# Performance work log

Measured on AMD Instinct MI355X. Metric: run time of the kernel, lower is better.

Reference implementation:

```python
import jax, jax.numpy as jnp
import numpy as np

B, N, C, H = 8, 1024, 1024, 16
D = C // H
DFF = 4 * C
EPS = 1e-6


def _ln(x):
    mu = jnp.mean(x, axis=-1, keepdims=True)
    var = jnp.mean(jnp.square(x - mu), axis=-1, keepdims=True)
    return (x - mu) / jnp.sqrt(var + EPS)


def _modulate(x, shift, scale):
    return x * (1 + scale) + shift


def setup_inputs() -> dict:
    key = jax.random.key(0)
    ks = jax.random.split(key, 12)
    s = 0.02
    inp = {
        "x": jax.random.normal(ks[0], (B, N, C), jnp.float32),
        "c": jax.random.normal(ks[1], (B, 1, C), jnp.float32),
        "causal_mask": jnp.tril(jnp.ones((N, N), jnp.int32))[None, None],  # [1,1,N,N]
        "qkv_w": jax.random.normal(ks[2], (3 * C, C), jnp.float32) * s,
        "qkv_b": jnp.zeros((3 * C,), jnp.float32),
        "proj_w": jax.random.normal(ks[3], (C, C), jnp.float32) * s,
        "proj_b": jnp.zeros((C,), jnp.float32),
        "fc1_w": jax.random.normal(ks[4], (DFF, C), jnp.float32) * s,
        "fc1_b": jnp.zeros((DFF,), jnp.float32),
        "fc2_w": jax.random.normal(ks[5], (C, DFF), jnp.float32) * s,
        "fc2_b": jnp.zeros((C,), jnp.float32),
        "ada_w": jax.random.normal(ks[6], (6 * C, C), jnp.float32) * s,
        "ada_b": jnp.zeros((6 * C,), jnp.float32),
    }
    return inp


def reference(x, c, causal_mask, qkv_w, qkv_b, proj_w, proj_b,
              fc1_w, fc1_b, fc2_w, fc2_b, ada_w, ada_b):
    # adaLN modulation: SiLU -> Linear(C -> 6C) -> chunk 6
    mod = jax.nn.silu(c) @ ada_w.T + ada_b  # [B,1,6C]
    (shift_msa, scale_msa, gate_msa,
     shift_mlp, scale_mlp, gate_mlp) = jnp.split(mod, 6, axis=-1)

    # --- causal attention ---
    y = _modulate(_ln(x), shift_msa, scale_msa)  # [B,N,C]
    qkv = y @ qkv_w.T + qkv_b                    # [B,N,3C]
    qkv = qkv.reshape(B, N, 3, H, D).transpose(2, 0, 3, 1, 4)  # [3,B,H,N,D]
    q, k, v = qkv[0], qkv[1], qkv[2]
    scale = D ** -0.5
    attn = jnp.einsum('bhnd,bhmd->bhnm', q, k) * scale  # [B,H,N,N]
    attn = jnp.where(causal_mask == 0, -jnp.inf, attn)
    attn = jax.nn.softmax(attn, axis=-1)
    o = jnp.einsum('bhnm,bhmd->bhnd', attn, v)
    o = o.transpose(0, 2, 1, 3).reshape(B, N, C)
    o = o @ proj_w.T + proj_b
    x = x + gate_msa * o

    # --- MLP ---
    z = _modulate(_ln(x), shift_mlp, scale_mlp)
    h = jax.nn.gelu(z @ fc1_w.T + fc1_b, approximate=True)
    m = h @ fc2_w.T + fc2_b
    x = x + gate_mlp * m
    return x
```

## Files before the change

kernel.cpp:

```cpp
#include <hip/hip_runtime.h>
#include <math.h>
#include <stdint.h>
#include <stddef.h>

namespace {

constexpr int kB = 8, kN = 1024, kC = 1024, kH = 16, kD = 64, kDFF = 4096;
constexpr int kM = kB * kN;
constexpr int k6C = 6 * kC;
constexpr float kQKScale = 0.18033688011112042f;
constexpr float kM8 = 8.0f;

typedef _Float16 half8 __attribute__((ext_vector_type(8)));
typedef _Float16 half4v __attribute__((ext_vector_type(4)));
typedef float f32x4 __attribute__((ext_vector_type(4)));
typedef int v4i __attribute__((ext_vector_type(4)));
typedef signed char i8;

__device__ inline void ld_lds16(const void* g, void* l) {
  __builtin_amdgcn_global_load_lds(
      (const __attribute__((address_space(1))) void*)g,
      (__attribute__((address_space(3))) void*)l, 16, 0, 0);
}

__device__ inline int xcd_swizzle(int flat, int nwg) {
  return (flat & 7) * (nwg >> 3) + (flat >> 3);
}

__device__ inline unsigned pack4_i8(float y0, float y1, float y2, float y3, float inv) {
  int q0 = (int)rintf(y0 * inv), q1 = (int)rintf(y1 * inv);
  int q2 = (int)rintf(y2 * inv), q3 = (int)rintf(y3 * inv);
  q0 = min(max(q0, -127), 127); q1 = min(max(q1, -127), 127);
  q2 = min(max(q2, -127), 127); q3 = min(max(q3, -127), 127);
  return (unsigned)(q0 & 0xFF) | ((unsigned)(q1 & 0xFF) << 8) |
         ((unsigned)(q2 & 0xFF) << 16) | ((unsigned)(q3 & 0xFF) << 24);
}

__global__ void cvt_f32_f16(const float* __restrict__ src, _Float16* __restrict__ dst) {
  size_t i = (size_t)blockIdx.x * 256 + threadIdx.x;
  float4 f = ((const float4*)src)[i];
  half4v h;
  h[0] = (_Float16)f.x; h[1] = (_Float16)f.y; h[2] = (_Float16)f.z; h[3] = (_Float16)f.w;
  ((half4v*)dst)[i] = h;
}

__global__ __launch_bounds__(256) void quant_w_kernel(
    const float* __restrict__ src, i8* __restrict__ dst, float* __restrict__ wscale) {
  int n = blockIdx.x, tid = threadIdx.x;
  const float* row = src + (size_t)n * kC;
  float4 f = ((const float4*)row)[tid];
  float m = fmaxf(fmaxf(fabsf(f.x), fabsf(f.y)), fmaxf(fabsf(f.z), fabsf(f.w)));
#pragma unroll
  for (int msk = 32; msk; msk >>= 1) m = fmaxf(m, __shfl_xor(m, msk));
  __shared__ float red[4];
  int w = tid >> 6, lane = tid & 63;
  if (lane == 0) red[w] = m;
  __syncthreads();
  m = fmaxf(fmaxf(red[0], red[1]), fmaxf(red[2], red[3]));
  m = fmaxf(m, 1e-12f);
  float inv = 127.f / m;
  ((unsigned*)(dst + (size_t)n * kC))[tid] = pack4_i8(f.x, f.y, f.z, f.w, inv);
  if (tid == 0) wscale[n] = m * (1.f / 127.f);
}

__global__ __launch_bounds__(256) void mod_kernel(
    const float* __restrict__ c, const float* __restrict__ ada_w,
    const float* __restrict__ ada_b, float* __restrict__ mod) {
  __shared__ float sc[kC];
  int b  = blockIdx.x / (k6C / 4);
  int j0 = (blockIdx.x % (k6C / 4)) * 4;
  int tid = threadIdx.x;
  for (int i = tid; i < kC; i += 256) {
    float v = c[b * kC + i];
    sc[i] = v / (1.f + expf(-v));
  }
  __syncthreads();
  int w = tid >> 6, lane = tid & 63;
  int j = j0 + w;
  const float* wr = ada_w + (size_t)j * kC;
  float acc = 0.f;
#pragma unroll
  for (int kk = 0; kk < kC / 64; ++kk) {
    int k = kk * 64 + lane;
    acc += sc[k] * wr[k];
  }
#pragma unroll
  for (int m = 32; m; m >>= 1) acc += __shfl_xor(acc, m);
  if (lane == 0) mod[b * k6C + j] = acc + ada_b[j];
}

template <typename T>
__global__ __launch_bounds__(256) void ln_mod_q_kernel(
    const T* __restrict__ x, const float* __restrict__ mod,
    i8* __restrict__ out, float* __restrict__ ascale,
    int shift_off, int scale_off) {
  int row = blockIdx.x;
  int b = row >> 10;
  const T* xr = x + (size_t)row * kC;
  int tid = threadIdx.x;
  int cc0 = tid * 4;
  float v[4];
  float s = 0.f, s2 = 0.f;
#pragma unroll
  for (int i = 0; i < 4; ++i) {
    v[i] = (float)xr[cc0 + i];
    s += v[i];
    s2 += v[i] * v[i];
  }
#pragma unroll
  for (int m = 32; m; m >>= 1) { s += __shfl_xor(s, m); s2 += __shfl_xor(s2, m); }
  __shared__ float red[8];
  __shared__ float redm[4];
  int w = tid >> 6, lane = tid & 63;
  if (lane == 0) { red[w] = s; red[4 + w] = s2; }
  __syncthreads();
  s  = red[0] + red[1] + red[2] + red[3];
  s2 = red[4] + red[5] + red[6] + red[7];
  float mu   = s * (1.f / kC);
  float var  = s2 * (1.f / kC) - mu * mu;
  float rstd = rsqrtf(var + 1e-6f);
  const float* mb = mod + (size_t)b * k6C;
  float y[4];
  float m = 0.f;
#pragma unroll
  for (int i = 0; i < 4; ++i) {
    y[i] = (v[i] - mu) * rstd * (1.f + mb[scale_off + cc0 + i]) + mb[shift_off + cc0 + i];
    m = fmaxf(m, fabsf(y[i]));
  }
#pragma unroll
  for (int msk = 32; msk; msk >>= 1) m = fmaxf(m, __shfl_xor(m, msk));
  if (lane == 0) redm[w] = m;
  __syncthreads();
  m = fmaxf(fmaxf(redm[0], redm[1]), fmaxf(redm[2], redm[3]));
  m = fmaxf(m, 1e-12f);
  float inv = 127.f / m;
  ((unsigned*)(out + (size_t)row * kC))[tid] = pack4_i8(y[0], y[1], y[2], y[3], inv);
  if (tid == 0) ascale[row] = m * (1.f / 127.f);
}

template <int EPI>
__global__ __launch_bounds__(256, 4) void gemm_i8_kernel(
    const i8* __restrict__ A, const i8* __restrict__ W,
    const float* __restrict__ ascale, const float* __restrict__ wscale,
    const float* __restrict__ bias, _Float16* __restrict__ outp,
    int M, int Nn, int K) {
  __shared__ __align__(16) i8 S[2 * 2 * 128 * 64];
  int tid = threadIdx.x;
  int nwg = (int)(gridDim.x * gridDim.y);
  int swz = xcd_swizzle((int)(blockIdx.y * gridDim.x + blockIdx.x), nwg);
  int bn = swz % (int)gridDim.x, bm = swz / (int)gridDim.x;
  int lane = tid & 63, w = tid >> 6;
  int l15 = lane & 15, quad = lane >> 4;
  int wr = (w >> 1) * 64, wc = (w & 1) * 64;

  v4i acc[4][4];
#pragma unroll
  for (int i = 0; i < 4; ++i)
#pragma unroll
    for (int j = 0; j < 4; ++j) acc[i][j] = (v4i){0, 0, 0, 0};

  const i8* Ag = A + (size_t)bm * 128 * K;
  const i8* Wg = W + (size_t)bn * 128 * K;
  int rg = lane >> 2;
  int gsl = lane & 3;

  int nk = K >> 6;
  {
    i8* As0 = S;
    i8* Bs0 = S + 128 * 64;
#pragma unroll
    for (int s = 0; s < 2; ++s) {
      int row = w * 32 + s * 16 + rg;
      int gc = (gsl ^ ((row >> 1) & 3)) * 16;
      ld_lds16(&Ag[(size_t)row * K + gc], &As0[(w * 32 + s * 16) * 64]);
      ld_lds16(&Wg[(size_t)row * K + gc], &Bs0[(w * 32 + s * 16) * 64]);
    }
  }
  __syncthreads();

  int cread = (quad ^ ((l15 >> 1) & 3)) * 16;
  for (int t = 0; t < nk; ++t) {
    const i8* As = S + (t & 1) * (2 * 128 * 64);
    const i8* Bs = As + 128 * 64;
    if (t + 1 < nk) {
      i8* Asn = S + ((t + 1) & 1) * (2 * 128 * 64);
      i8* Bsn = Asn + 128 * 64;
      int kt = (t + 1) << 6;
#pragma unroll
      for (int s = 0; s < 2; ++s) {
        int row = w * 32 + s * 16 + rg;
        int gc = (gsl ^ ((row >> 1) & 3)) * 16;
        ld_lds16(&Ag[(size_t)row * K + kt + gc], &Asn[(w * 32 + s * 16) * 64]);
        ld_lds16(&Wg[(size_t)row * K + kt + gc], &Bsn[(w * 32 + s * 16) * 64]);
      }
    }
    v4i af[4], bf[4];
#pragma unroll
    for (int i = 0; i < 4; ++i)
      af[i] = *(const v4i*)&As[(wr + i * 16 + l15) * 64 + cread];
#pragma unroll
    for (int j = 0; j < 4; ++j)
      bf[j] = *(const v4i*)&Bs[(wc + j * 16 + l15) * 64 + cread];
#pragma unroll
    for (int i = 0; i < 4; ++i)
#pragma unroll
      for (int j = 0; j < 4; ++j)
        acc[i][j] = __builtin_amdgcn_mfma_i32_16x16x64_i8(af[i], bf[j], acc[i][j], 0, 0, 0);
    __syncthreads();
  }

  _Float16* Cs = (_Float16*)S;
  int row0 = wr + quad * 4;
  int col0 = wc + l15;
#pragma unroll
  for (int i = 0; i < 4; ++i) {
#pragma unroll
    for (int j = 0; j < 4; ++j) {
      int colL = col0 + j * 16;
      int n = bn * 128 + colL;
      float ws = wscale[n];
      float bv = bias[n];
#pragma unroll
      for (int r = 0; r < 4; ++r) {
        int rowL = row0 + i * 16 + r;
        float as = ascale[bm * 128 + rowL];
        float v = (float)acc[i][j][r] * (as * ws) + bv;
        if constexpr (EPI == 0) {
          if (n < kC) v *= kQKScale;
        } else {
          float u = v + 0.044715f * v * v * v;
          float t = exp2f(-2.302208f * u);
          v = v * __builtin_amdgcn_rcpf(1.f + t);
        }
        Cs[rowL * 128 + (((colL >> 3) ^ (rowL & 7)) << 3) + (colL & 7)] = (_Float16)v;
      }
    }
  }
  __syncthreads();
#pragma unroll
  for (int p = 0; p < 8; ++p) {
    int r = (tid >> 4) + p * 16;
    int cc = tid & 15;
    half8 hv = *(const half8*)&Cs[r * 128 + ((cc ^ (r & 7)) << 3)];
    size_t gm = (size_t)(bm * 128 + r);
    int coff = bn * 128 + cc * 8;
    *(half8*)&outp[gm * Nn + coff] = hv;
  }
}

template <int EPI>
__global__ __launch_bounds__(256) void gemm_f16_kernel(
    const _Float16* __restrict__ A, const _Float16* __restrict__ W,
    const float* __restrict__ bias, void* __restrict__ outp,
    const void* __restrict__ resid, const float* __restrict__ mod,
    int M, int Nn, int K, int gate_off) {
  __shared__ __align__(16) _Float16 S[2 * 2 * 128 * 64];
  int tid = threadIdx.x;
  int nwg = (int)(gridDim.x * gridDim.y);
  int swz = xcd_swizzle((int)(blockIdx.y * gridDim.x + blockIdx.x), nwg);
  int bn = swz % (int)gridDim.x, bm = swz / (int)gridDim.x;
  int lane = tid & 63, w = tid >> 6;
  int l15 = lane & 15, quad = lane >> 4;
  int wr = (w >> 1) * 64, wc = (w & 1) * 64;

  f32x4 acc[4][4];
#pragma unroll
  for (int i = 0; i < 4; ++i)
#pragma unroll
    for (int j = 0; j < 4; ++j) acc[i][j] = (f32x4){0.f, 0.f, 0.f, 0.f};

  const _Float16* Ag = A + (size_t)bm * 128 * K;
  const _Float16* Wg = W + (size_t)bn * 128 * K;
  int r8 = lane >> 3;
  int jc = ((lane & 7) ^ r8) * 8;

  int nk = K / 64;
  {
    _Float16* Asp = S;
    _Float16* Bsp = S + 128 * 64;
#pragma unroll
    for (int u = 0; u < 4; ++u) {
      int row = w * 32 + u * 8 + r8;
      ld_lds16(&Ag[(size_t)row * K + jc], &Asp[(w * 32 + u * 8) * 64]);
      ld_lds16(&Wg[(size_t)row * K + jc], &Bsp[(w * 32 + u * 8) * 64]);
    }
  }
  __syncthreads();

  for (int t = 0; t < nk; ++t) {
    const _Float16* As = S + (t & 1) * (2 * 128 * 64);
    const _Float16* Bs = As + 128 * 64;
    if (t + 1 < nk) {
      _Float16* Asn = S + ((t + 1) & 1) * (2 * 128 * 64);
      _Float16* Bsn = Asn + 128 * 64;
      int kt = (t + 1) * 64;
#pragma unroll
      for (int u = 0; u < 4; ++u) {
        int row = w * 32 + u * 8 + r8;
        ld_lds16(&Ag[(size_t)row * K + kt + jc], &Asn[(w * 32 + u * 8) * 64]);
        ld_lds16(&Wg[(size_t)row * K + kt + jc], &Bsn[(w * 32 + u * 8) * 64]);
      }
    }
#pragma unroll
    for (int kk = 0; kk < 2; ++kk) {
      half8 af[4], bf[4];
#pragma unroll
      for (int i = 0; i < 4; ++i)
        af[i] = *(const half8*)&As[(wr + i * 16 + l15) * 64 +
                                   (((kk * 4 + quad) ^ (l15 & 7)) * 8)];
#pragma unroll
      for (int j = 0; j < 4; ++j)
        bf[j] = *(const half8*)&Bs[(wc + j * 16 + l15) * 64 +
                                   (((kk * 4 + quad) ^ (l15 & 7)) * 8)];
#pragma unroll
      for (int i = 0; i < 4; ++i)
#pragma unroll
        for (int j = 0; j < 4; ++j)
          acc[i][j] = __builtin_amdgcn_mfma_f32_16x16x32_f16(af[i], bf[j], acc[i][j], 0, 0, 0);
    }
    __syncthreads();
  }

  _Float16* Cs = S;
  int row0 = wr + quad * 4;
  int col0 = wc + l15;
#pragma unroll
  for (int i = 0; i < 4; ++i) {
#pragma unroll
    for (int j = 0; j < 4; ++j) {
      int colL = col0 + j * 16;
      int n = bn * 128 + colL;
      float bv = bias[n];
#pragma unroll
      for (int r = 0; r < 4; ++r) {
        int rowL = row0 + i * 16 + r;
        float v = acc[i][j][r] + bv;
        Cs[rowL * 128 + (((colL >> 3) ^ (rowL & 7)) << 3) + (colL & 7)] = (_Float16)v;
      }
    }
  }
  __syncthreads();
  int b6 = (bm >> 3) * k6C + gate_off + bn * 128;
#pragma unroll
  for (int p = 0; p < 8; ++p) {
    int r = (tid >> 4) + p * 16;
    int cc = tid & 15;
    half8 hv = *(const half8*)&Cs[r * 128 + ((cc ^ (r & 7)) << 3)];
    size_t gm = (size_t)(bm * 128 + r);
    int coff = bn * 128 + cc * 8;
    if constexpr (EPI == 2) {
      const float* rp = &((const float*)resid)[gm * kC + coff];
      const float* gp = &mod[b6 + cc * 8];
      half8 ov;
#pragma unroll
      for (int e = 0; e < 8; ++e) ov[e] = (_Float16)(rp[e] + gp[e] * (float)hv[e]);
      *(half8*)&((_Float16*)outp)[gm * kC + coff] = ov;
    } else {
      const _Float16* rp = &((const _Float16*)resid)[gm * kC + coff];
      const float* gp = &mod[b6 + cc * 8];
      half8 rv = *(const half8*)rp;
      float ov[8];
#pragma unroll
      for (int e = 0; e < 8; ++e) ov[e] = (float)rv[e] + gp[e] * (float)hv[e];
      *(float4*)&((float*)outp)[gm * kC + coff] = *(float4*)&ov[0];
      *(float4*)&((float*)outp)[gm * kC + coff + 4] = *(float4*)&ov[4];
    }
  }
}

__global__ __launch_bounds__(256) void vtrans_kernel(
    const _Float16* __restrict__ qkv, _Float16* __restrict__ vT) {
  int nt = blockIdx.x, h = blockIdx.y, b = blockIdx.z;
  __shared__ _Float16 Ts[64 * 72];
  int tid = threadIdx.x;
  const _Float16* src = qkv + ((size_t)(b * kN + nt * 64)) * (3 * kC) + 2 * kC + h * 64;
#pragma unroll
  for (int u = 0; u < 2; ++u) {
    int idx = tid + u * 256;
    int r = idx >> 3, c8 = (idx & 7) * 8;
    *(uint4*)&Ts[r * 72 + c8] = *(const uint4*)&src[(size_t)r * (3 * kC) + c8];
  }
  __syncthreads();
  _Float16* dst = vT + (((size_t)(b * kH + h)) * 64) * kN + nt * 64;
#pragma unroll
  for (int u = 0; u < 2; ++u) {
    int idx = tid + u * 256;
    int d = idx >> 3, n8 = (idx & 7) * 8;
    half8 v;
#pragma unroll
    for (int e = 0; e < 8; ++e) v[e] = Ts[(n8 + e) * 72 + d];
    *(half8*)&dst[(size_t)d * kN + n8] = v;
  }
}

__global__ __launch_bounds__(256) void attn_kernel(
    const _Float16* __restrict__ qkv, const _Float16* __restrict__ vT,
    _Float16* __restrict__ o) {
  int nwg = (int)(gridDim.x * gridDim.y * gridDim.z);
  int flat = (int)((blockIdx.z * gridDim.y + blockIdx.y) * gridDim.x + blockIdx.x);
  int swz = xcd_swizzle(flat, nwg);
  int qt = swz % (int)gridDim.x;
  int tmp = swz / (int)gridDim.x;
  int h = tmp % (int)gridDim.y, b = tmp / (int)gridDim.y;
  __shared__ __align__(16) _Float16 Qs[128 * 64];
  __shared__ __align__(16) _Float16 Ks[64 * 64];
  __shared__ __align__(16) _Float16 Vs[64 * 64];
  __shared__ __align__(16) _Float16 Ps[128 * 72];
  int tid = threadIdx.x, lane = tid & 63, w = tid >> 6;
  int l15 = lane & 15, quad = lane >> 4;
  int wq = w * 32;
  int r8 = lane >> 3;
  int jc = ((lane & 7) ^ r8) * 8;

  const _Float16* Qg = qkv + ((size_t)(b * kN + qt * 128)) * (3 * kC) + h * kD;
  const _Float16* Kg = qkv + ((size_t)(b * kN)) * (3 * kC) + kC + h * kD;
  const _Float16* Vg = vT + ((size_t)(b * kH + h) * kD) * kN;

#pragma unroll
  for (int u = 0; u < 4; ++u)
    ld_lds16(&Qg[(size_t)(w * 32 + u * 8 + r8) * (3 * kC) + jc],
             &Qs[(w * 32 + u * 8) * 64]);
  __syncthreads();

  half8 aq[2][2];
#pragma unroll
  for (int i = 0; i < 2; ++i)
#pragma unroll
    for (int kk = 0; kk < 2; ++kk)
      aq[i][kk] = *(const half8*)&Qs[(wq + i * 16 + l15) * 64 +
                                     (((kk * 4 + quad) ^ (l15 & 7)) * 8)];

  f32x4 o_acc[2][4];
  f32x4 lsum[2];
#pragma unroll
  for (int i = 0; i < 2; ++i) {
    lsum[i] = (f32x4){0.f, 0.f, 0.f, 0.f};
#pragma unroll
    for (int dt = 0; dt < 4; ++dt) o_acc[i][dt] = (f32x4){0.f, 0.f, 0.f, 0.f};
  }
  half8 ones;
#pragma unroll
  for (int e = 0; e < 8; ++e) ones[e] = (_Float16)1.f;

  int jmax = 2 * qt + 2;
  for (int j = 0; j < jmax; ++j) {
#pragma unroll
    for (int u = 0; u < 2; ++u) {
      int row = w * 16 + u * 8 + r8;
      ld_lds16(&Kg[(size_t)(j * 64 + row) * (3 * kC) + jc], &Ks[(w * 16 + u * 8) * 64]);
      ld_lds16(&Vg[(size_t)row * kN + j * 64 + jc],         &Vs[(w * 16 + u * 8) * 64]);
    }
    __syncthreads();
    bool need_mask = (j >= 2 * qt);

    f32x4 s[2][4];
#pragma unroll
    for (int ct = 0; ct < 4; ++ct) {
      half8 b0 = *(const half8*)&Ks[(ct * 16 + l15) * 64 + ((quad ^ (l15 & 7)) * 8)];
      half8 b1 = *(const half8*)&Ks[(ct * 16 + l15) * 64 + (((4 + quad) ^ (l15 & 7)) * 8)];
#pragma unroll
      for (int i = 0; i < 2; ++i) {
        f32x4 t = (f32x4){0.f, 0.f, 0.f, 0.f};
        t = __builtin_amdgcn_mfma_f32_16x16x32_f16(aq[i][0], b0, t, 0, 0, 0);
        t = __builtin_amdgcn_mfma_f32_16x16x32_f16(aq[i][1], b1, t, 0, 0, 0);
        s[i][ct] = t;
      }
    }

#pragma unroll
    for (int i = 0; i < 2; ++i)
#pragma unroll
      for (int ct = 0; ct < 4; ++ct)
#pragma unroll
        for (int r = 0; r < 4; ++r) {
          float p = exp2f(fminf(s[i][ct][r] - kM8, 14.f));
          if (need_mask) {
            int kg = j * 64 + ct * 16 + l15;
            int qg = qt * 128 + wq + i * 16 + quad * 4 + r;
            if (kg > qg) p = 0.f;
          }
          Ps[(wq + i * 16 + quad * 4 + r) * 72 + ct * 16 + l15] = (_Float16)p;
        }

    half8 ap[2][2];
#pragma unroll
    for (int i = 0; i < 2; ++i) {
      ap[i][0] = *(const half8*)&Ps[(wq + i * 16 + l15) * 72 + quad * 8];
      ap[i][1] = *(const half8*)&Ps[(wq + i * 16 + l15) * 72 + 32 + quad * 8];
      lsum[i] = __builtin_amdgcn_mfma_f32_16x16x32_f16(ap[i][0], ones, lsum[i], 0, 0, 0);
      lsum[i] = __builtin_amdgcn_mfma_f32_16x16x32_f16(ap[i][1], ones, lsum[i], 0, 0, 0);
    }
#pragma unroll
    for (int dt = 0; dt < 4; ++dt) {
      half8 bv0 = *(const half8*)&Vs[(dt * 16 + l15) * 64 + ((quad ^ (l15 & 7)) * 8)];
      half8 bv1 = *(const half8*)&Vs[(dt * 16 + l15) * 64 + (((4 + quad) ^ (l15 & 7)) * 8)];
#pragma unroll
      for (int i = 0; i < 2; ++i) {
        o_acc[i][dt] = __builtin_amdgcn_mfma_f32_16x16x32_f16(ap[i][0], bv0, o_acc[i][dt], 0, 0, 0);
        o_acc[i][dt] = __builtin_amdgcn_mfma_f32_16x16x32_f16(ap[i][1], bv1, o_acc[i][dt], 0, 0, 0);
      }
    }
    __syncthreads();
  }

#pragma unroll
  for (int i = 0; i < 2; ++i) {
    float rl[4];
#pragma unroll
    for (int r = 0; r < 4; ++r) rl[r] = __builtin_amdgcn_rcpf(lsum[i][r]);
#pragma unroll
    for (int dt = 0; dt < 4; ++dt)
#pragma unroll
      for (int r = 0; r < 4; ++r) {
        int q = qt * 128 + wq + i * 16 + quad * 4 + r;
        o[((size_t)(b * kN + q)) * kC + h * kD + dt * 16 + l15] =
            (_Float16)(o_acc[i][dt][r] * rl[r]);
      }
  }
}

}

extern "C" void kernel_launch(void* const* d_in, const int* in_sizes, int n_in,
                              void* d_out, int out_size, void* d_ws, size_t ws_size,
                              hipStream_t stream) {
  const float* x      = (const float*)d_in[0];
  const float* c      = (const float*)d_in[1];
  const float* qkv_w  = (const float*)d_in[3];
  const float* qkv_b  = (const float*)d_in[4];
  const float* proj_w = (const float*)d_in[5];
  const float* proj_b = (const float*)d_in[6];
  const float* fc1_w  = (const float*)d_in[7];
  const float* fc1_b  = (const float*)d_in[8];
  const float* fc2_w  = (const float*)d_in[9];
  const float* fc2_b  = (const float*)d_in[10];
  const float* ada_w  = (const float*)d_in[11];
  const float* ada_b  = (const float*)d_in[12];
  float* out = (float*)d_out;

  char* ws = (char*)d_ws;
  float*    mod     = (float*)(ws);
  i8*       w_qkv   = (i8*)(ws + 196608);
  i8*       w_fc1   = (i8*)(ws + 3342336);
  _Float16* w_proj  = (_Float16*)(ws + 7536640);
  _Float16* w_fc2   = (_Float16*)(ws + 9633792);
  i8*       bufA    = (i8*)(ws + 18022400);
  float*    ascale  = (float*)(ws + 26411008);
  float*    ws_qkv  = (float*)(ws + 26443776);
  float*    ws_fc1  = (float*)(ws + 26456064);
  _Float16* vT      = (_Float16*)(ws + 26509312);
  _Float16* x2h     = (_Float16*)(ws + 26509312);
  _Float16* bufO    = (_Float16*)(ws + 43286528);
  _Float16* qkvh    = (_Float16*)(ws + 60063744);
  _Float16* hbuf    = (_Float16*)(ws + 60063744);

  quant_w_kernel<<<3 * kC, 256, 0, stream>>>(qkv_w, w_qkv, ws_qkv);
  quant_w_kernel<<<kDFF, 256, 0, stream>>>(fc1_w, w_fc1, ws_fc1);
  cvt_f32_f16<<<kC * kC / 1024, 256, 0, stream>>>(proj_w, w_proj);
  cvt_f32_f16<<<kC * kDFF / 1024, 256, 0, stream>>>(fc2_w, w_fc2);
  mod_kernel<<<kB * (k6C / 4), 256, 0, stream>>>(c, ada_w, ada_b, mod);
  ln_mod_q_kernel<float><<<kM, 256, 0, stream>>>(x, mod, bufA, ascale, 0, kC);
  gemm_i8_kernel<0><<<dim3(3 * kC / 128, kM / 128), 256, 0, stream>>>(
      bufA, w_qkv, ascale, ws_qkv, qkv_b, qkvh, kM, 3 * kC, kC);
  vtrans_kernel<<<dim3(kN / 64, kH, kB), 256, 0, stream>>>(qkvh, vT);
  attn_kernel<<<dim3(kN / 128, kH, kB), 256, 0, stream>>>(qkvh, vT, bufO);
  gemm_f16_kernel<2><<<dim3(kC / 128, kM / 128), 256, 0, stream>>>(
      bufO, w_proj, proj_b, x2h, x, mod, kM, kC, kC, 2 * kC);
  ln_mod_q_kernel<_Float16><<<kM, 256, 0, stream>>>(x2h, mod, bufA, ascale, 3 * kC, 4 * kC);
  gemm_i8_kernel<1><<<dim3(kDFF / 128, kM / 128), 256, 0, stream>>>(
      bufA, w_fc1, ascale, ws_fc1, fc1_b, hbuf, kM, kDFF, kC);
  gemm_f16_kernel<3><<<dim3(kC / 128, kM / 128), 256, 0, stream>>>(
      hbuf, w_fc2, fc2_b, out, x2h, mod, kM, kC, kDFF, 5 * kC);
}
```

Measured before the change: 465.2 us.

## Prefetch two K-tiles ahead in GEMM with register-staged fragments

Restructures the GEMM main loop so that two K-tiles are in flight. Each iteration waits on vmcnt for the current tile and loads all A/B fragments for the tile into registers. It then passes a barrier and issues the global-to-LDS load for tile t+2 into the freed buffer before running the MFMAs. This lets the next loads overlap with the matrix math and replaces the end-of-iteration syncthreads. The cost is more VGPRs for the double fragment set and a reliance on manual waitcnt counts being correct.

```diff
diff --git a/kernel.cpp b/kernel.cpp
--- a/kernel.cpp
+++ b/kernel.cpp
@@ -274,51 +274,56 @@
   int r8 = lane >> 3;
   int jc = ((lane & 7) ^ r8) * 8;
 
-  int nk = K / 64;
-  {
-    _Float16* Asp = S;
-    _Float16* Bsp = S + 128 * 64;
+  auto stage = [&](int buf, int kt) {
+    _Float16* Asn = S + buf * (2 * 128 * 64);
+    _Float16* Bsn = Asn + 128 * 64;
 #pragma unroll
     for (int u = 0; u < 4; ++u) {
       int row = w * 32 + u * 8 + r8;
-      ld_lds16(&Ag[(size_t)row * K + jc], &Asp[(w * 32 + u * 8) * 64]);
-      ld_lds16(&Wg[(size_t)row * K + jc], &Bsp[(w * 32 + u * 8) * 64]);
-    }
-  }
-  __syncthreads();
+      ld_lds16(&Ag[(size_t)row * K + kt + jc], &Asn[(w * 32 + u * 8) * 64]);
+      ld_lds16(&Wg[(size_t)row * K + kt + jc], &Bsn[(w * 32 + u * 8) * 64]);
+    }
+  };
+
+  int nk = K / 64;
+  stage(0, 0);
+  stage(1, 64);
 
   for (int t = 0; t < nk; ++t) {
+    if (t + 1 < nk) {
+      asm volatile("s_waitcnt vmcnt(8)" ::: "memory");
+    } else {
+      asm volatile("s_waitcnt vmcnt(0)" ::: "memory");
+    }
+    __builtin_amdgcn_s_barrier();
+    __builtin_amdgcn_sched_barrier(0);
     const _Float16* As = S + (t & 1) * (2 * 128 * 64);
     const _Float16* Bs = As + 128 * 64;
-    if (t + 1 < nk) {
-      _Float16* Asn = S + ((t + 1) & 1) * (2 * 128 * 64);
-      _Float16* Bsn = Asn + 128 * 64;
-      int kt = (t + 1) * 64;
-#pragma unroll
-      for (int u = 0; u < 4; ++u) {
-        int row = w * 32 + u * 8 + r8;
-        ld_lds16(&Ag[(size_t)row * K + kt + jc], &Asn[(w * 32 + u * 8) * 64]);
-        ld_lds16(&Wg[(size_t)row * K + kt + jc], &Bsn[(w * 32 + u * 8) * 64]);
-      }
-    }
+    half8 af[2][4], bf[2][4];
 #pragma unroll
     for (int kk = 0; kk < 2; ++kk) {
-      half8 af[4], bf[4];
 #pragma unroll
       for (int i = 0; i < 4; ++i)
-        af[i] = *(const half8*)&As[(wr + i * 16 + l15) * 64 +
-                                   (((kk * 4 + quad) ^ (l15 & 7)) * 8)];
+        af[kk][i] = *(const half8*)&As[(wr + i * 16 + l15) * 64 +
+                                       (((kk * 4 + quad) ^ (l15 & 7)) * 8)];
 #pragma unroll
       for (int j = 0; j < 4; ++j)
-        bf[j] = *(const half8*)&Bs[(wc + j * 16 + l15) * 64 +
-                                   (((kk * 4 + quad) ^ (l15 & 7)) * 8)];
+        bf[kk][j] = *(const half8*)&Bs[(wc + j * 16 + l15) * 64 +
+                                       (((kk * 4 + quad) ^ (l15 & 7)) * 8)];
+    }
+    asm volatile("s_waitcnt lgkmcnt(0)" ::: "memory");
+    __builtin_amdgcn_sched_barrier(0);
+    __builtin_amdgcn_s_barrier();
+    __builtin_amdgcn_sched_barrier(0);
+    if (t + 2 < nk) stage(t & 1, (t + 2) * 64);
+#pragma unroll
+    for (int kk = 0; kk < 2; ++kk)
 #pragma unroll
       for (int i = 0; i < 4; ++i)
 #pragma unroll
         for (int j = 0; j < 4; ++j)
-          acc[i][j] = __builtin_amdgcn_mfma_f32_16x16x32_f16(af[i], bf[j], acc[i][j], 0, 0, 0);
-    }
-    __syncthreads();
+          acc[i][j] = __builtin_amdgcn_mfma_f32_16x16x32_f16(af[kk][i], bf[kk][j],
+                                                             acc[i][j], 0, 0, 0);
   }
 
   _Float16* Cs = S;
```

Result: no change. 467.3 us (+0.4%).
